# Performance work log

Hardware: AMD Instinct MI355X
Metric: run time of the kernel (lower is better)

Reference implementation:

```python
import jax, jax.numpy as jnp
import numpy as np

B, T, N, C, D = 8, 12, 1024, 64, 10

def setup_inputs() -> dict:
    key = jax.random.key(0)
    ks = jax.random.split(key, 7)
    x = jax.random.normal(ks[0], (B, T, N, C), dtype=jnp.float32)
    e1 = jax.random.normal(ks[1], (N, D), dtype=jnp.float32)
    e2 = jax.random.normal(ks[2], (N, D), dtype=jnp.float32)
    # buffer: sym-normalized adjacency after the __init__-time softmax
    A_sym = jax.random.uniform(ks[3], (N, N), dtype=jnp.float32)
    weights_pool = jax.random.normal(ks[4], (N, C, C), dtype=jnp.float32) * 0.02
    bias_pool = jax.random.normal(ks[5], (N, C), dtype=jnp.float32) * 0.02
    alpha = jnp.array([0.9], dtype=jnp.float32)
    beta = jnp.array([0.9], dtype=jnp.float32)
    gamma = jnp.array([0.1], dtype=jnp.float32)
    return {"x": x, "node_embeddings1": e1, "node_embeddings2": e2,
            "A_sym": A_sym, "weights_pool": weights_pool, "bias_pool": bias_pool,
            "alpha": alpha, "beta": beta, "gamma": gamma}


def reference(x, node_embeddings1, node_embeddings2, A_sym, weights_pool,
              bias_pool, alpha, beta, gamma):
    n = node_embeddings1.shape[0]
    # dynamic supports: relu(tanh(E1 E2^T - E2 E1^T)) + I
    s = jnp.tanh(node_embeddings1 @ node_embeddings2.T
                 - node_embeddings2 @ node_embeddings1.T)
    supports = jnp.eye(n, dtype=x.dtype) + jax.nn.relu(s)          # (N,N)

    # static branch: row-softmax of the precomputed sym-norm adjacency
    A = jax.nn.softmax(A_sym, axis=-1)                              # (N,N)
    x_static = jax.nn.relu(jnp.einsum('nm,btmc->btnc', A, x))       # (B,T,N,C)

    # spatial attention branch (note: softmax over the TIME axis, as in source)
    score = jnp.einsum('btnc,btmc->btnm', x, x)                     # (B,T,N,N)
    score = jax.nn.softmax(score, axis=1)
    x_sa = jax.nn.relu(jnp.einsum('btnm,btmc->btnc', score, x))     # (B,T,N,C)

    # adaptive graph conv: per-node weights/bias from supports
    weights = jnp.einsum('nd,dio->nio', supports, weights_pool)     # (N,C,C)
    bias = supports @ bias_pool                                     # (N,C)
    x_g = jnp.einsum('nm,btmc->btnc', supports, x)                  # (B,T,N,C)
    x_gconv = jax.nn.relu(jnp.einsum('btni,nio->btno', x_g, weights) + bias)

    return alpha * x_gconv + beta * x_sa + gamma * x_static
```

## Files before the change

kernel.cpp:

```cpp
#include <hip/hip_runtime.h>
#include <math.h>

#define Bdim 8
#define Tdim 12
#define BT   96
#define Ndim 1024
#define Cdim 64
#define Ddim 10
#define Jdim 6144
#define IOdim 4096

typedef __attribute__((ext_vector_type(4))) float f32x4;
typedef __attribute__((ext_vector_type(8))) short bf16x8;

__device__ inline short f2bf(float f) {
    union { float f; unsigned u; } v; v.f = f;
    return (short)((v.u + 0x8000u) >> 16);
}
__device__ inline float bf2f(short s) {
    union { float f; unsigned u; } v; v.u = ((unsigned)(unsigned short)s) << 16;
    return v.f;
}
__device__ inline void load_lds16(const void* g, void* l) {
    __builtin_amdgcn_global_load_lds(
        (const __attribute__((address_space(1))) unsigned int*)g,
        (__attribute__((address_space(3))) unsigned int*)l, 16, 0, 0);
}
__device__ inline float fexp(float x) { return __expf(x); }
__device__ inline float frcp(float x) { return __builtin_amdgcn_rcpf(x); }
__device__ inline float flog(float x) { return __logf(x); }

__global__ __launch_bounds__(256) void k_supports(
    const float* __restrict__ e1, const float* __restrict__ e2,
    short* __restrict__ Sbf)
{
    int idx = blockIdx.x * 256 + threadIdx.x;
    int i = idx >> 10, j = idx & 1023;
    float s = 0.f;
#pragma unroll
    for (int d = 0; d < Ddim; ++d)
        s += e1[i * Ddim + d] * e2[j * Ddim + d]
           - e2[i * Ddim + d] * e1[j * Ddim + d];
    float t = 1.f - 2.f * frcp(fexp(2.f * s) + 1.f);
    float v = fmaxf(t, 0.f);
    if (i == j) v += 1.f;
    Sbf[idx] = f2bf(v);
}

__global__ __launch_bounds__(256) void k_softmax_rows(
    const float* __restrict__ In, short* __restrict__ Out)
{
    int row = blockIdx.x;
    const float* r = In + (size_t)row * Ndim;
    short* o = Out + (size_t)row * Ndim;
    __shared__ float red[256];
    int tid = threadIdx.x;
    float vals[4];
    float lmax = -INFINITY;
#pragma unroll
    for (int i = 0; i < 4; ++i) { vals[i] = r[tid + 256 * i]; lmax = fmaxf(lmax, vals[i]); }
    red[tid] = lmax; __syncthreads();
    for (int s = 128; s > 0; s >>= 1) {
        if (tid < s) red[tid] = fmaxf(red[tid], red[tid + s]);
        __syncthreads();
    }
    float m = red[0]; __syncthreads();
    float lsum = 0.f;
#pragma unroll
    for (int i = 0; i < 4; ++i) { vals[i] = fexp(vals[i] - m); lsum += vals[i]; }
    red[tid] = lsum; __syncthreads();
    for (int s = 128; s > 0; s >>= 1) {
        if (tid < s) red[tid] += red[tid + s];
        __syncthreads();
    }
    float inv = frcp(red[0]);
#pragma unroll
    for (int i = 0; i < 4; ++i) o[tid + 256 * i] = f2bf(vals[i] * inv);
}

__global__ __launch_bounds__(256) void k_cvt_x(
    const float* __restrict__ x, short* __restrict__ xbf, short* __restrict__ xT)
{
    __shared__ float Lt[64][65];
    int bt = blockIdx.y, n0 = blockIdx.x * 64;
    const float* src = x + (size_t)bt * 65536 + (size_t)n0 * 64;
    int tid = threadIdx.x;
#pragma unroll
    for (int p = 0; p < 4; ++p) {
        int idx = p * 256 + tid;
        int r = idx >> 4, c4 = idx & 15;
        float4 v = *(const float4*)&src[r * 64 + c4 * 4];
        short4 s4 = make_short4(f2bf(v.x), f2bf(v.y), f2bf(v.z), f2bf(v.w));
        *(short4*)&xbf[(size_t)bt * 65536 + (size_t)(n0 + r) * 64 + c4 * 4] = s4;
        Lt[r][c4 * 4 + 0] = v.x; Lt[r][c4 * 4 + 1] = v.y;
        Lt[r][c4 * 4 + 2] = v.z; Lt[r][c4 * 4 + 3] = v.w;
    }
    __syncthreads();
#pragma unroll
    for (int p = 0; p < 4; ++p) {
        int idx = p * 256 + tid;
        int c = idx >> 4, k4 = idx & 15;
        short4 s4 = make_short4(f2bf(Lt[k4 * 4 + 0][c]), f2bf(Lt[k4 * 4 + 1][c]),
                                f2bf(Lt[k4 * 4 + 2][c]), f2bf(Lt[k4 * 4 + 3][c]));
        *(short4*)&xT[(size_t)bt * 65536 + (size_t)c * 1024 + n0 + k4 * 4] = s4;
    }
}

__global__ __launch_bounds__(256) void k_cvt_wp(
    const float* __restrict__ wp, short* __restrict__ wpT)
{
    __shared__ float Lt[64][65];
    int k0 = blockIdx.y * 64, j0 = blockIdx.x * 64;
    int tid = threadIdx.x;
#pragma unroll
    for (int p = 0; p < 4; ++p) {
        int idx = p * 256 + tid;
        int r = idx >> 4, c4 = idx & 15;
        float4 v = *(const float4*)&wp[(size_t)(k0 + r) * IOdim + j0 + c4 * 4];
        Lt[r][c4 * 4 + 0] = v.x; Lt[r][c4 * 4 + 1] = v.y;
        Lt[r][c4 * 4 + 2] = v.z; Lt[r][c4 * 4 + 3] = v.w;
    }
    __syncthreads();
#pragma unroll
    for (int p = 0; p < 4; ++p) {
        int idx = p * 256 + tid;
        int c = idx >> 4, k4 = idx & 15;
        short4 s4 = make_short4(f2bf(Lt[k4 * 4 + 0][c]), f2bf(Lt[k4 * 4 + 1][c]),
                                f2bf(Lt[k4 * 4 + 2][c]), f2bf(Lt[k4 * 4 + 3][c]));
        *(short4*)&wpT[(size_t)(j0 + c) * 1024 + k0 + k4 * 4] = s4;
    }
}

__global__ __launch_bounds__(256) void k_cvt_bp(
    const float* __restrict__ bp, short* __restrict__ bpT)
{
    __shared__ float Lt[64][65];
    int k0 = blockIdx.x * 64;
    int tid = threadIdx.x;
#pragma unroll
    for (int p = 0; p < 4; ++p) {
        int idx = p * 256 + tid;
        int r = idx >> 4, c4 = idx & 15;
        float4 v = *(const float4*)&bp[(size_t)(k0 + r) * 64 + c4 * 4];
        Lt[r][c4 * 4 + 0] = v.x; Lt[r][c4 * 4 + 1] = v.y;
        Lt[r][c4 * 4 + 2] = v.z; Lt[r][c4 * 4 + 3] = v.w;
    }
    __syncthreads();
#pragma unroll
    for (int p = 0; p < 4; ++p) {
        int idx = p * 256 + tid;
        int c = idx >> 4, k4 = idx & 15;
        short4 s4 = make_short4(f2bf(Lt[k4 * 4 + 0][c]), f2bf(Lt[k4 * 4 + 1][c]),
                                f2bf(Lt[k4 * 4 + 2][c]), f2bf(Lt[k4 * 4 + 3][c]));
        *(short4*)&bpT[(size_t)c * 1024 + k0 + k4 * 4] = s4;
    }
}

template<int MODE>
__global__ __launch_bounds__(256) void k_gemm_bt(
    const short* __restrict__ A, const short* __restrict__ Bm,
    float* __restrict__ Cf, short* __restrict__ Cb,
    const float* __restrict__ gamma_p)
{
    __shared__ short At[128 * 64];
    __shared__ short Bt[128 * 64];
    const int tid = threadIdx.x;
    const int w = tid >> 6, l = tid & 63;
    const int l15 = l & 15, q = l >> 4;
    const int n0 = blockIdx.x * 128, j0 = blockIdx.y * 128;
    const int wr = (w & 1) * 64, wc = (w >> 1) * 64;
    const int lrow = l >> 3, lc8 = l & 7;

    f32x4 acc[4][4];
#pragma unroll
    for (int i = 0; i < 4; ++i)
#pragma unroll
        for (int j = 0; j < 4; ++j) acc[i][j] = (f32x4)0.f;

    for (int k0 = 0; k0 < 1024; k0 += 64) {
        __syncthreads();
#pragma unroll
        for (int p = 0; p < 4; ++p) {
            int r = p * 32 + w * 8 + lrow;
            int sc = lc8 ^ (r & 7);
            load_lds16(A + (size_t)(n0 + r) * 1024 + k0 + sc * 8,
                       &At[(p * 32 + w * 8) * 64]);
            load_lds16(Bm + (size_t)(j0 + r) * 1024 + k0 + sc * 8,
                       &Bt[(p * 32 + w * 8) * 64]);
        }
        __syncthreads();
#pragma unroll
        for (int ks = 0; ks < 2; ++ks) {
            bf16x8 af[4], bf[4];
#pragma unroll
            for (int rt = 0; rt < 4; ++rt) {
                int row = wr + rt * 16 + l15;
                int pos = (ks * 4 + q) ^ (row & 7);
                af[rt] = *(const bf16x8*)&At[row * 64 + pos * 8];
            }
#pragma unroll
            for (int ct = 0; ct < 4; ++ct) {
                int row = wc + ct * 16 + l15;
                int pos = (ks * 4 + q) ^ (row & 7);
                bf[ct] = *(const bf16x8*)&Bt[row * 64 + pos * 8];
            }
#pragma unroll
            for (int rt = 0; rt < 4; ++rt)
#pragma unroll
                for (int ct = 0; ct < 4; ++ct)
                    acc[rt][ct] = __builtin_amdgcn_mfma_f32_16x16x32_bf16(
                        af[rt], bf[ct], acc[rt][ct], 0, 0, 0);
        }
    }

    float gmm = (MODE == 0) ? gamma_p[0] : 0.f;
#pragma unroll
    for (int rt = 0; rt < 4; ++rt) {
        int nr = n0 + wr + rt * 16 + q * 4;
#pragma unroll
        for (int ct = 0; ct < 4; ++ct) {
            int j = j0 + wc + ct * 16 + l15;
#pragma unroll
            for (int r = 0; r < 4; ++r) {
                float v = acc[rt][ct][r];
                int n = nr + r;
                if (MODE == 1) {
                    Cb[(size_t)n * IOdim + j] = f2bf(v);
                } else if (n < 1024) {
                    int bt = j >> 6, c = j & 63;
                    Cf[(size_t)bt * 65536 + (size_t)n * 64 + c] = gmm * fmaxf(v, 0.f);
                } else {
                    Cb[(size_t)(n - 1024) * Jdim + j] = f2bf(v);
                }
            }
        }
    }
}

__global__ __launch_bounds__(256, 4) void k_sa_z(
    const short* __restrict__ xbf, float* __restrict__ Lout)
{
    __shared__ short Xn[64 * 64];
    __shared__ short Xm[64 * 64];

    int id = blockIdx.x;
    int b = id & 7;
    int r = id >> 3;
    int tn = r & 15, tm = r >> 4;
    int tid = threadIdx.x;
    int w = tid >> 6, l = tid & 63;
    int l15 = l & 15, q = l >> 4;
    int lrow = l >> 3, lc8 = l & 7;
    int n0 = tn * 64, m0 = tm * 64;
    int wn = (w & 1) * 32, wm = (w >> 1) * 32;

    const short* Xb = xbf + (size_t)b * Tdim * Ndim * Cdim;
    float* Lb = Lout + ((size_t)b << 20);

    f32x4 M[2][2], Z[2][2];
#pragma unroll
    for (int nh = 0; nh < 2; ++nh)
#pragma unroll
        for (int mh = 0; mh < 2; ++mh) { M[nh][mh] = (f32x4)(-INFINITY); Z[nh][mh] = (f32x4)0.f; }

    for (int t = 0; t < Tdim; ++t) {
        const short* xt = Xb + (size_t)t * (Ndim * Cdim);
        __syncthreads();
#pragma unroll
        for (int p = 0; p < 2; ++p) {
            int rr = p * 32 + w * 8 + lrow;
            int sc = lc8 ^ (rr & 7);
            load_lds16(xt + (size_t)(n0 + rr) * 64 + sc * 8, &Xn[(p * 32 + w * 8) * 64]);
            load_lds16(xt + (size_t)(m0 + rr) * 64 + sc * 8, &Xm[(p * 32 + w * 8) * 64]);
        }
        __syncthreads();

        f32x4 sacc[2][2];
        sacc[0][0] = (f32x4)0.f; sacc[0][1] = (f32x4)0.f;
        sacc[1][0] = (f32x4)0.f; sacc[1][1] = (f32x4)0.f;
#pragma unroll
        for (int ch = 0; ch < 2; ++ch) {
            bf16x8 qb[2], af[2];
#pragma unroll
            for (int nh = 0; nh < 2; ++nh) {
                int row = wn + nh * 16 + l15;
                int pos = (ch * 4 + q) ^ (row & 7);
                qb[nh] = *(const bf16x8*)&Xn[row * 64 + pos * 8];
            }
#pragma unroll
            for (int mh = 0; mh < 2; ++mh) {
                int row = wm + mh * 16 + l15;
                int pos = (ch * 4 + q) ^ (row & 7);
                af[mh] = *(const bf16x8*)&Xm[row * 64 + pos * 8];
            }
#pragma unroll
            for (int nh = 0; nh < 2; ++nh)
#pragma unroll
                for (int mh = 0; mh < 2; ++mh)
                    sacc[nh][mh] = __builtin_amdgcn_mfma_f32_16x16x32_bf16(
                        af[mh], qb[nh], sacc[nh][mh], 0, 0, 0);
        }
#pragma unroll
        for (int nh = 0; nh < 2; ++nh)
#pragma unroll
            for (int mh = 0; mh < 2; ++mh)
#pragma unroll
                for (int i = 0; i < 4; ++i) {
                    float s  = sacc[nh][mh][i];
                    float mo = M[nh][mh][i];
                    float mn = fmaxf(mo, s);
                    Z[nh][mh][i] = Z[nh][mh][i] * fexp(mo - mn) + fexp(s - mn);
                    M[nh][mh][i] = mn;
                }
    }
#pragma unroll
    for (int nh = 0; nh < 2; ++nh)
#pragma unroll
        for (int mh = 0; mh < 2; ++mh) {
            f32x4 e;
#pragma unroll
            for (int i = 0; i < 4; ++i)
                e[i] = M[nh][mh][i] + flog(Z[nh][mh][i]);
            *(f32x4*)&Lb[(size_t)(n0 + wn + nh * 16 + l15) * 1024
                         + m0 + wm + mh * 16 + q * 4] = e;
        }
}

__global__ __launch_bounds__(256, 4) void k_sa_pv(
    const short* __restrict__ xbf, const short* __restrict__ xT,
    const float* __restrict__ Lsum, float* __restrict__ Out,
    const float* __restrict__ beta_p)
{
    __shared__ short Xm[32 * 72];
    __shared__ short XTl[64 * 40];
    __shared__ short Pl[4][16][40];

    int id = blockIdx.x;
    int b = id & 7;
    int r = id >> 3;
    int nt = r & 7, t = r >> 3;
    int tid = threadIdx.x;
    int w = tid >> 6, l = tid & 63;
    int l15 = l & 15, q = l >> 4;
    int n0 = nt * 128 + w * 32;

    const short* Xb  = xbf + ((size_t)b * Tdim + t) * (Ndim * Cdim);
    const short* XTb = xT  + ((size_t)b * Tdim + t) * (Ndim * Cdim);
    const float* Lb  = Lsum + ((size_t)b << 20);

    int srow  = tid >> 3, sc8 = tid & 7;
    int srow2 = tid >> 2, sc4 = tid & 3;

    bf16x8 qf[2][2];
#pragma unroll
    for (int nh = 0; nh < 2; ++nh)
#pragma unroll
        for (int ch = 0; ch < 2; ++ch)
            qf[nh][ch] = *(const bf16x8*)&Xb[(n0 + nh * 16 + l15) * 64 + ch * 32 + q * 8];

    f32x4 oacc[2][4];
#pragma unroll
    for (int nh = 0; nh < 2; ++nh)
#pragma unroll
        for (int ct = 0; ct < 4; ++ct) oacc[nh][ct] = (f32x4)0.f;

    for (int mi = 0; mi < 32; ++mi) {
        int m0 = mi * 32;
        __syncthreads();
        bf16x8 v  = *(const bf16x8*)&Xb[(size_t)(m0 + srow) * 64 + sc8 * 8];
        bf16x8 v2 = *(const bf16x8*)&XTb[(size_t)srow2 * 1024 + m0 + sc4 * 8];
        f32x4 e[2][2];
#pragma unroll
        for (int nh = 0; nh < 2; ++nh)
#pragma unroll
            for (int mh = 0; mh < 2; ++mh)
                e[nh][mh] = *(const f32x4*)&Lb[(size_t)(n0 + nh * 16 + l15) * 1024
                                               + m0 + mh * 16 + q * 4];
        *(bf16x8*)&Xm[srow * 72 + sc8 * 8]   = v;
        *(bf16x8*)&XTl[srow2 * 40 + sc4 * 8] = v2;
        __syncthreads();

        f32x4 sacc[2][2];
        sacc[0][0] = (f32x4)0.f; sacc[0][1] = (f32x4)0.f;
        sacc[1][0] = (f32x4)0.f; sacc[1][1] = (f32x4)0.f;
#pragma unroll
        for (int ch = 0; ch < 2; ++ch) {
#pragma unroll
            for (int mh = 0; mh < 2; ++mh) {
                bf16x8 af = *(const bf16x8*)&Xm[(mh * 16 + l15) * 72 + ch * 32 + q * 8];
                sacc[0][mh] = __builtin_amdgcn_mfma_f32_16x16x32_bf16(
                    af, qf[0][ch], sacc[0][mh], 0, 0, 0);
                sacc[1][mh] = __builtin_amdgcn_mfma_f32_16x16x32_bf16(
                    af, qf[1][ch], sacc[1][mh], 0, 0, 0);
            }
        }
#pragma unroll
        for (int nh = 0; nh < 2; ++nh) {
#pragma unroll
            for (int mh = 0; mh < 2; ++mh) {
                f32x4 p = sacc[nh][mh];
                f32x4 ee = e[nh][mh];
                unsigned u0 = (unsigned)(unsigned short)f2bf(fexp(p[0] - ee[0]))
                            | ((unsigned)(unsigned short)f2bf(fexp(p[1] - ee[1])) << 16);
                unsigned u1 = (unsigned)(unsigned short)f2bf(fexp(p[2] - ee[2]))
                            | ((unsigned)(unsigned short)f2bf(fexp(p[3] - ee[3])) << 16);
                *(uint2*)&Pl[w][l15][mh * 16 + q * 4] = make_uint2(u0, u1);
            }
            bf16x8 pf = *(const bf16x8*)&Pl[w][l15][q * 8];
#pragma unroll
            for (int ct = 0; ct < 4; ++ct) {
                bf16x8 bfr = *(const bf16x8*)&XTl[(ct * 16 + l15) * 40 + q * 8];
                oacc[nh][ct] = __builtin_amdgcn_mfma_f32_16x16x32_bf16(
                    pf, bfr, oacc[nh][ct], 0, 0, 0);
            }
        }
    }

    float beta = beta_p[0];
#pragma unroll
    for (int nh = 0; nh < 2; ++nh)
#pragma unroll
        for (int ct = 0; ct < 4; ++ct)
#pragma unroll
            for (int r2 = 0; r2 < 4; ++r2) {
                size_t idx = (((size_t)b * Tdim + t) * Ndim + n0 + nh * 16 + q * 4 + r2) * Cdim
                           + ct * 16 + l15;
                Out[idx] += beta * fmaxf(oacc[nh][ct][r2], 0.f);
            }
}

__global__ __launch_bounds__(256) void k_bias(
    const short* __restrict__ Sbf, const short* __restrict__ bpT,
    float* __restrict__ bias)
{
    int tid = threadIdx.x;
    int w = tid >> 6, l = tid & 63;
    int l15 = l & 15, q = l >> 4;
    int nr = blockIdx.x * 64 + w * 16;

    f32x4 acc[4];
#pragma unroll
    for (int ct = 0; ct < 4; ++ct) acc[ct] = (f32x4)0.f;

    for (int k0 = 0; k0 < 1024; k0 += 32) {
        bf16x8 af = *(const bf16x8*)&Sbf[(size_t)(nr + l15) * 1024 + k0 + q * 8];
#pragma unroll
        for (int ct = 0; ct < 4; ++ct) {
            bf16x8 bf = *(const bf16x8*)&bpT[(size_t)(ct * 16 + l15) * 1024 + k0 + q * 8];
            acc[ct] = __builtin_amdgcn_mfma_f32_16x16x32_bf16(af, bf, acc[ct], 0, 0, 0);
        }
    }
#pragma unroll
    for (int ct = 0; ct < 4; ++ct)
#pragma unroll
        for (int r = 0; r < 4; ++r)
            bias[(size_t)(nr + q * 4 + r) * 64 + ct * 16 + l15] = acc[ct][r];
}

__global__ __launch_bounds__(384) void k_gconv(
    const short* __restrict__ xgT, const short* __restrict__ Wb,
    const float* __restrict__ bias, float* __restrict__ Out,
    const float* __restrict__ alpha_p)
{
    __shared__ short Wl[64 * 64];
    int n = blockIdx.x;
    int tid = threadIdx.x;
    for (int f = tid; f < 512; f += 384) {
        int k = f >> 3, j = f & 7;
        *(bf16x8*)&Wl[k * 64 + (j ^ ((k >> 3) & 7)) * 8] =
            *(const bf16x8*)&Wb[(size_t)n * IOdim + f * 8];
    }
    __syncthreads();
    int w = tid / 64, l = tid & 63, l15 = l & 15, q = l >> 4;
    f32x4 acc[4];
#pragma unroll
    for (int ct = 0; ct < 4; ++ct) acc[ct] = (f32x4)0.f;
    const short* xr = xgT + (size_t)n * Jdim + (size_t)(w * 16 + l15) * 64;
#pragma unroll
    for (int ks = 0; ks < 2; ++ks) {
        bf16x8 a = *(const bf16x8*)&xr[ks * 32 + q * 8];
        int kb = ks * 32 + q * 8;
        int msk = (kb >> 3) & 7;
#pragma unroll
        for (int ct = 0; ct < 4; ++ct) {
            bf16x8 bfr;
#pragma unroll
            for (int e = 0; e < 8; ++e) {
                int o = ct * 16 + l15;
                bfr[e] = Wl[(kb + e) * 64 + (((o >> 3) ^ msk) * 8) + (o & 7)];
            }
            acc[ct] = __builtin_amdgcn_mfma_f32_16x16x32_bf16(a, bfr, acc[ct], 0, 0, 0);
        }
    }
    float alpha = alpha_p[0];
#pragma unroll
    for (int ct = 0; ct < 4; ++ct) {
        int o = ct * 16 + l15;
        float bo = bias[(size_t)n * 64 + o];
#pragma unroll
        for (int r = 0; r < 4; ++r) {
            int bt = w * 16 + q * 4 + r;
            size_t idx = (size_t)bt * 65536 + (size_t)n * 64 + o;
            Out[idx] += alpha * fmaxf(acc[ct][r] + bo, 0.f);
        }
    }
}

extern "C" void kernel_launch(void* const* d_in, const int* in_sizes, int n_in,
                              void* d_out, int out_size, void* d_ws, size_t ws_size,
                              hipStream_t stream)
{
    const float* x     = (const float*)d_in[0];
    const float* e1    = (const float*)d_in[1];
    const float* e2    = (const float*)d_in[2];
    const float* Asym  = (const float*)d_in[3];
    const float* wpool = (const float*)d_in[4];
    const float* bpool = (const float*)d_in[5];
    const float* alpha = (const float*)d_in[6];
    const float* beta  = (const float*)d_in[7];
    const float* gamma = (const float*)d_in[8];
    float* out = (float*)d_out;

    short* ASbf = (short*)d_ws;
    short* xbf  = ASbf + 2048 * 1024;
    short* xT   = xbf  + 6291456;
    short* wpT  = xT   + 6291456;
    short* Wbf  = wpT  + 4194304;
    short* xgT  = Wbf  + 4194304;
    float* bias = (float*)(xgT + 6291456);
    float* Lsum = bias + 65536;
    short* bpT  = (short*)(Lsum + 8388608);

    k_supports<<<4096, 256, 0, stream>>>(e1, e2, ASbf + 1024 * 1024);
    k_softmax_rows<<<1024, 256, 0, stream>>>(Asym, ASbf);
    k_cvt_x<<<dim3(16, 96), 256, 0, stream>>>(x, xbf, xT);
    k_cvt_wp<<<dim3(64, 16), 256, 0, stream>>>(wpool, wpT);
    k_cvt_bp<<<16, 256, 0, stream>>>(bpool, bpT);
    k_sa_z<<<2048, 256, 0, stream>>>(xbf, Lsum);
    k_gemm_bt<0><<<dim3(16, 48), 256, 0, stream>>>(ASbf, xT, out, xgT, gamma);
    k_gemm_bt<1><<<dim3(8, 32), 256, 0, stream>>>(ASbf + 1024 * 1024, wpT, nullptr, Wbf, nullptr);
    k_bias<<<16, 256, 0, stream>>>(ASbf + 1024 * 1024, bpT, bias);
    k_sa_pv<<<768, 256, 0, stream>>>(xbf, xT, Lsum, out, beta);
    k_gconv<<<1024, 384, 0, stream>>>(xgT, Wbf, bias, out, alpha);
}
```

Baseline: 319.3 us.

## Enlarge time-softmax normalizer tiles and store log-sum in fp16

The time-axis softmax normalizer kernel now uses 128x128 output tiles with 512-thread blocks instead of 64x64 tiles with 256 threads. Each loaded x tile is reused across more MFMA work, which reduces redundant global loads across the 12 time steps. The per-(b,n,m) log-sum-exp buffer is stored as fp16 instead of fp32, halving the traffic written by the normalizer kernel and read back by the PV kernel. The fp16 storage of the log normalizer costs some precision in the exponentials and could also overflow if scores get large. Register use also rises with the 4x2 accumulator arrays.

```diff
diff --git a/kernel.cpp b/kernel.cpp
--- a/kernel.cpp
+++ b/kernel.cpp
@@ -12,6 +12,7 @@
 
 typedef __attribute__((ext_vector_type(4))) float f32x4;
 typedef __attribute__((ext_vector_type(8))) short bf16x8;
+typedef __attribute__((ext_vector_type(4))) _Float16 f16x4;
 
 __device__ inline short f2bf(float f) {
     union { float f; unsigned u; } v; v.f = f;
@@ -237,29 +238,29 @@
     }
 }
 
-__global__ __launch_bounds__(256, 4) void k_sa_z(
-    const short* __restrict__ xbf, float* __restrict__ Lout)
-{
-    __shared__ short Xn[64 * 64];
-    __shared__ short Xm[64 * 64];
+__global__ __launch_bounds__(512, 2) void k_sa_z(
+    const short* __restrict__ xbf, short* __restrict__ Lh)
+{
+    __shared__ short Xn[128 * 64];
+    __shared__ short Xm[128 * 64];
 
     int id = blockIdx.x;
     int b = id & 7;
     int r = id >> 3;
-    int tn = r & 15, tm = r >> 4;
+    int tn = r & 7, tm = r >> 3;
     int tid = threadIdx.x;
     int w = tid >> 6, l = tid & 63;
     int l15 = l & 15, q = l >> 4;
     int lrow = l >> 3, lc8 = l & 7;
-    int n0 = tn * 64, m0 = tm * 64;
-    int wn = (w & 1) * 32, wm = (w >> 1) * 32;
+    int n0 = tn * 128, m0 = tm * 128;
+    int wn = (w & 1) * 64, wm = (w >> 1) * 32;
 
     const short* Xb = xbf + (size_t)b * Tdim * Ndim * Cdim;
-    float* Lb = Lout + ((size_t)b << 20);
-
-    f32x4 M[2][2], Z[2][2];
-#pragma unroll
-    for (int nh = 0; nh < 2; ++nh)
+    short* Lb = Lh + ((size_t)b << 20);
+
+    f32x4 M[4][2], Z[4][2];
+#pragma unroll
+    for (int nh = 0; nh < 4; ++nh)
 #pragma unroll
         for (int mh = 0; mh < 2; ++mh) { M[nh][mh] = (f32x4)(-INFINITY); Z[nh][mh] = (f32x4)0.f; }
 
@@ -268,21 +269,23 @@
         __syncthreads();
 #pragma unroll
         for (int p = 0; p < 2; ++p) {
-            int rr = p * 32 + w * 8 + lrow;
+            int rr = p * 64 + w * 8 + lrow;
             int sc = lc8 ^ (rr & 7);
-            load_lds16(xt + (size_t)(n0 + rr) * 64 + sc * 8, &Xn[(p * 32 + w * 8) * 64]);
-            load_lds16(xt + (size_t)(m0 + rr) * 64 + sc * 8, &Xm[(p * 32 + w * 8) * 64]);
-        }
-        __syncthreads();
-
-        f32x4 sacc[2][2];
-        sacc[0][0] = (f32x4)0.f; sacc[0][1] = (f32x4)0.f;
-        sacc[1][0] = (f32x4)0.f; sacc[1][1] = (f32x4)0.f;
+            load_lds16(xt + (size_t)(n0 + rr) * 64 + sc * 8, &Xn[(p * 64 + w * 8) * 64]);
+            load_lds16(xt + (size_t)(m0 + rr) * 64 + sc * 8, &Xm[(p * 64 + w * 8) * 64]);
+        }
+        __syncthreads();
+
+        f32x4 sacc[4][2];
+#pragma unroll
+        for (int nh = 0; nh < 4; ++nh)
+#pragma unroll
+            for (int mh = 0; mh < 2; ++mh) sacc[nh][mh] = (f32x4)0.f;
 #pragma unroll
         for (int ch = 0; ch < 2; ++ch) {
-            bf16x8 qb[2], af[2];
-#pragma unroll
-            for (int nh = 0; nh < 2; ++nh) {
+            bf16x8 qb[4], af[2];
+#pragma unroll
+            for (int nh = 0; nh < 4; ++nh) {
                 int row = wn + nh * 16 + l15;
                 int pos = (ch * 4 + q) ^ (row & 7);
                 qb[nh] = *(const bf16x8*)&Xn[row * 64 + pos * 8];
@@ -294,14 +297,14 @@
                 af[mh] = *(const bf16x8*)&Xm[row * 64 + pos * 8];
             }
 #pragma unroll
-            for (int nh = 0; nh < 2; ++nh)
+            for (int nh = 0; nh < 4; ++nh)
 #pragma unroll
                 for (int mh = 0; mh < 2; ++mh)
                     sacc[nh][mh] = __builtin_amdgcn_mfma_f32_16x16x32_bf16(
                         af[mh], qb[nh], sacc[nh][mh], 0, 0, 0);
         }
 #pragma unroll
-        for (int nh = 0; nh < 2; ++nh)
+        for (int nh = 0; nh < 4; ++nh)
 #pragma unroll
             for (int mh = 0; mh < 2; ++mh)
 #pragma unroll
@@ -314,21 +317,21 @@
                 }
     }
 #pragma unroll
-    for (int nh = 0; nh < 2; ++nh)
+    for (int nh = 0; nh < 4; ++nh)
 #pragma unroll
         for (int mh = 0; mh < 2; ++mh) {
-            f32x4 e;
+            f16x4 ev;
 #pragma unroll
             for (int i = 0; i < 4; ++i)
-                e[i] = M[nh][mh][i] + flog(Z[nh][mh][i]);
-            *(f32x4*)&Lb[(size_t)(n0 + wn + nh * 16 + l15) * 1024
-                         + m0 + wm + mh * 16 + q * 4] = e;
+                ev[i] = (_Float16)(M[nh][mh][i] + flog(Z[nh][mh][i]));
+            *(f16x4*)&Lb[(size_t)(n0 + wn + nh * 16 + l15) * 1024
+                         + m0 + wm + mh * 16 + q * 4] = ev;
         }
 }
 
 __global__ __launch_bounds__(256, 4) void k_sa_pv(
     const short* __restrict__ xbf, const short* __restrict__ xT,
-    const float* __restrict__ Lsum, float* __restrict__ Out,
+    const short* __restrict__ Lh, float* __restrict__ Out,
     const float* __restrict__ beta_p)
 {
     __shared__ short Xm[32 * 72];
@@ -346,7 +349,7 @@
 
     const short* Xb  = xbf + ((size_t)b * Tdim + t) * (Ndim * Cdim);
     const short* XTb = xT  + ((size_t)b * Tdim + t) * (Ndim * Cdim);
-    const float* Lb  = Lsum + ((size_t)b << 20);
+    const short* Lb  = Lh + ((size_t)b << 20);
 
     int srow  = tid >> 3, sc8 = tid & 7;
     int srow2 = tid >> 2, sc4 = tid & 3;
@@ -369,12 +372,12 @@
         __syncthreads();
         bf16x8 v  = *(const bf16x8*)&Xb[(size_t)(m0 + srow) * 64 + sc8 * 8];
         bf16x8 v2 = *(const bf16x8*)&XTb[(size_t)srow2 * 1024 + m0 + sc4 * 8];
-        f32x4 e[2][2];
+        f16x4 e[2][2];
 #pragma unroll
         for (int nh = 0; nh < 2; ++nh)
 #pragma unroll
             for (int mh = 0; mh < 2; ++mh)
-                e[nh][mh] = *(const f32x4*)&Lb[(size_t)(n0 + nh * 16 + l15) * 1024
+                e[nh][mh] = *(const f16x4*)&Lb[(size_t)(n0 + nh * 16 + l15) * 1024
                                                + m0 + mh * 16 + q * 4];
         *(bf16x8*)&Xm[srow * 72 + sc8 * 8]   = v;
         *(bf16x8*)&XTl[srow2 * 40 + sc4 * 8] = v2;
@@ -399,11 +402,11 @@
 #pragma unroll
             for (int mh = 0; mh < 2; ++mh) {
                 f32x4 p = sacc[nh][mh];
-                f32x4 ee = e[nh][mh];
-                unsigned u0 = (unsigned)(unsigned short)f2bf(fexp(p[0] - ee[0]))
-                            | ((unsigned)(unsigned short)f2bf(fexp(p[1] - ee[1])) << 16);
-                unsigned u1 = (unsigned)(unsigned short)f2bf(fexp(p[2] - ee[2]))
-                            | ((unsigned)(unsigned short)f2bf(fexp(p[3] - ee[3])) << 16);
+                f16x4 ee = e[nh][mh];
+                unsigned u0 = (unsigned)(unsigned short)f2bf(fexp(p[0] - (float)ee[0]))
+                            | ((unsigned)(unsigned short)f2bf(fexp(p[1] - (float)ee[1])) << 16);
+                unsigned u1 = (unsigned)(unsigned short)f2bf(fexp(p[2] - (float)ee[2]))
+                            | ((unsigned)(unsigned short)f2bf(fexp(p[3] - (float)ee[3])) << 16);
                 *(uint2*)&Pl[w][l15][mh * 16 + q * 4] = make_uint2(u0, u1);
             }
             bf16x8 pf = *(const bf16x8*)&Pl[w][l15][q * 8];
@@ -528,18 +531,18 @@
     short* Wbf  = wpT  + 4194304;
     short* xgT  = Wbf  + 4194304;
     float* bias = (float*)(xgT + 6291456);
-    float* Lsum = bias + 65536;
-    short* bpT  = (short*)(Lsum + 8388608);
+    short* Lh   = (short*)(bias + 65536);
+    short* bpT  = Lh + 8388608;
 
     k_supports<<<4096, 256, 0, stream>>>(e1, e2, ASbf + 1024 * 1024);
     k_softmax_rows<<<1024, 256, 0, stream>>>(Asym, ASbf);
     k_cvt_x<<<dim3(16, 96), 256, 0, stream>>>(x, xbf, xT);
     k_cvt_wp<<<dim3(64, 16), 256, 0, stream>>>(wpool, wpT);
     k_cvt_bp<<<16, 256, 0, stream>>>(bpool, bpT);
-    k_sa_z<<<2048, 256, 0, stream>>>(xbf, Lsum);
+    k_sa_z<<<512, 512, 0, stream>>>(xbf, Lh);
     k_gemm_bt<0><<<dim3(16, 48), 256, 0, stream>>>(ASbf, xT, out, xgT, gamma);
     k_gemm_bt<1><<<dim3(8, 32), 256, 0, stream>>>(ASbf + 1024 * 1024, wpT, nullptr, Wbf, nullptr);
     k_bias<<<16, 256, 0, stream>>>(ASbf + 1024 * 1024, bpT, bias);
-    k_sa_pv<<<768, 256, 0, stream>>>(xbf, xT, Lsum, out, beta);
+    k_sa_pv<<<768, 256, 0, stream>>>(xbf, xT, Lh, out, beta);
     k_gconv<<<1024, 384, 0, stream>>>(xgT, Wbf, bias, out, alpha);
 }
```

Result: slower. 334.6 us (+4.8%).
